# Kernel optimization log

Measured on AMD Instinct MI355X. Metric: run time of the kernel, lower is better.

Reference implementation:

```python
import jax, jax.numpy as jnp
import numpy as np

N_HEADS = 12
ROPE_THETA = 10000.0


def _rope(x, pos):
    # x: [B, H, S, hd]; rotate only first hd//2 channels (partial RoPE, dim=head_dim//2)
    rot = x.shape[-1] // 2
    inv_freq = 1.0 / (ROPE_THETA ** (jnp.arange(0, rot, 2, dtype=jnp.float32) / rot))  # [rot/2]
    freqs = pos[:, None] * inv_freq[None, :]          # [S, rot/2]
    freqs = jnp.repeat(freqs, 2, axis=-1)             # [S, rot] interleaved repeat
    cos = jnp.cos(freqs)
    sin = jnp.sin(freqs)
    x_rot, x_pass = x[..., :rot], x[..., rot:]
    xr = x_rot.reshape(x_rot.shape[:-1] + (rot // 2, 2))
    x_half = jnp.stack([-xr[..., 1], xr[..., 0]], axis=-1).reshape(x_rot.shape)
    x_rot = x_rot * cos + x_half * sin
    return jnp.concatenate([x_rot, x_pass], axis=-1)


def setup_inputs() -> dict:
    key = jax.random.key(0)
    ks = jax.random.split(key, 9)
    B, S, D = 2, 2048, 768
    x = jax.random.normal(ks[0], (B, S, D), dtype=jnp.float32)
    w = lambda k: jax.random.normal(k, (D, D), dtype=jnp.float32) * 0.02
    return {
        'x': x,
        'Wq': w(ks[1]), 'bq': jnp.zeros((D,), jnp.float32),
        'Wk': w(ks[2]), 'bk': jnp.zeros((D,), jnp.float32),
        'Wv': w(ks[3]), 'bv': jnp.zeros((D,), jnp.float32),
        'Wo': w(ks[4]), 'bo': jnp.zeros((D,), jnp.float32),
    }


def reference(x, Wq, bq, Wk, bk, Wv, bv, Wo, bo):
    B, S, D = x.shape
    H = N_HEADS
    hd = D // H
    # QKV projections (torch Linear: y = x W^T + b)
    q = (x @ Wq.T + bq).reshape(B, S, H, hd).transpose(0, 2, 1, 3)  # [B,H,S,hd]
    k = (x @ Wk.T + bk).reshape(B, S, H, hd).transpose(0, 2, 1, 3)
    v = (x @ Wv.T + bv).reshape(B, S, H, hd).transpose(0, 2, 1, 3)
    pos = jnp.arange(S, dtype=jnp.float32)
    q = _rope(q, pos)
    k = _rope(k, pos)
    scale = 1.0 / jnp.sqrt(jnp.asarray(hd, jnp.float32))
    scores = jnp.einsum('bhqd,bhkd->bhqk', q, k) * scale            # [B,H,S,S]
    causal = jnp.tril(jnp.ones((S, S), dtype=bool))
    scores = jnp.where(causal, scores, jnp.finfo(scores.dtype).min)
    attn = jax.nn.softmax(scores, axis=-1)
    out = jnp.einsum('bhqk,bhkd->bhqd', attn, v)                    # [B,H,S,hd]
    out = out.transpose(0, 2, 1, 3).reshape(B, S, D)
    return out @ Wo.T + bo
```

## Files before the change

kernel.cpp:

```cpp
#include <hip/hip_runtime.h>
#include <math.h>

#define S_  2048
#define D_  768
#define H_  12

typedef float f32x4 __attribute__((ext_vector_type(4)));
typedef __bf16 bf16x8 __attribute__((ext_vector_type(8)));
typedef unsigned short u16;

#define MFMA(a, b, c) __builtin_amdgcn_mfma_f32_16x16x32_bf16(a, b, c, 0, 0, 0)
#define LOG2E 1.44269504f

__device__ __forceinline__ u16 f2bf(float f) {
  union { float f; unsigned u; } c;
  c.f = f;
  unsigned r = c.u + 0x7FFFu + ((c.u >> 16) & 1u);
  return (u16)(r >> 16);
}

typedef const unsigned int __attribute__((address_space(1))) gu32;
typedef unsigned int __attribute__((address_space(3))) lu32;

__device__ __forceinline__ void gload_lds16(const void* g, void* l) {
  __builtin_amdgcn_global_load_lds((gu32*)g, (lu32*)l, 16, 0, 0);
}

__global__ __launch_bounds__(256) void trig_kernel(float2* __restrict__ trig) {
  int i = blockIdx.x * 256 + threadIdx.x;
  int s = i >> 4, p = i & 15;
  float inv = powf(10000.0f, -(float)p / 16.0f);
  float f = (float)s * inv;
  trig[i] = make_float2(cosf(f), sinf(f));
}

__global__ __launch_bounds__(256) void cvt_all(
    const float* __restrict__ x, const float* __restrict__ wq,
    const float* __restrict__ wk, const float* __restrict__ wv,
    const float* __restrict__ wo, u16* __restrict__ xb, u16* __restrict__ wqb,
    u16* __restrict__ wkb, u16* __restrict__ wvb, u16* __restrict__ wob) {
  int idx = blockIdx.x * 256 + threadIdx.x;
  const float4* src;
  u16* dst;
  int off;
  if (idx < 786432) {
    src = (const float4*)x; dst = xb; off = idx;
  } else {
    int r = idx - 786432;
    int sel = r / 147456;
    off = r - sel * 147456;
    src = (const float4*)(sel == 0 ? wq : sel == 1 ? wk : sel == 2 ? wv : wo);
    dst = sel == 0 ? wqb : sel == 1 ? wkb : sel == 2 ? wvb : wob;
  }
  float4 v = src[off];
  ushort4 h = make_ushort4(f2bf(v.x), f2bf(v.y), f2bf(v.z), f2bf(v.w));
  *(ushort4*)(dst + (size_t)off * 4) = h;
}

template <int MODE>
__global__ __launch_bounds__(256) void proj_mfma(
    const u16* __restrict__ A, const u16* __restrict__ Wb,
    const float* __restrict__ bias, void* __restrict__ dst,
    const float2* __restrict__ trig) {
  __shared__ u16 As[4096];
  __shared__ u16 Bs[4096];
  const int t = threadIdx.x;
  const int l = t & 63, w = t >> 6;
  const int wr = w >> 1, wc = w & 1;
  const int n0 = blockIdx.x * 64;
  const int m0 = blockIdx.y * 64;

  const f32x4 zero = {0.f, 0.f, 0.f, 0.f};
  f32x4 acc[2][2];
#pragma unroll
  for (int i = 0; i < 2; ++i)
#pragma unroll
    for (int j = 0; j < 2; ++j) acc[i][j] = zero;

  for (int k0 = 0; k0 < 768; k0 += 64) {
    __syncthreads();
#pragma unroll
    for (int rnd = 0; rnd < 2; ++rnd) {
      int id = t + rnd * 256;
      int r = id >> 3, c = id & 7;
      int cs = ((c ^ (r & 7)) << 3);
      gload_lds16(A + (size_t)(m0 + r) * 768 + k0 + cs,
                  &As[(w * 64 + rnd * 256) * 8]);
      gload_lds16(Wb + (size_t)(n0 + r) * 768 + k0 + cs,
                  &Bs[(w * 64 + rnd * 256) * 8]);
    }
    __syncthreads();

    bf16x8 af[2][2], bw[2][2];
#pragma unroll
    for (int mf = 0; mf < 2; ++mf)
#pragma unroll
      for (int kh = 0; kh < 2; ++kh) {
        int row = wr * 32 + mf * 16 + (l & 15);
        int ch = (kh * 4 + (l >> 4)) ^ (row & 7);
        af[mf][kh] = *(const bf16x8*)&As[row * 64 + ch * 8];
      }
#pragma unroll
    for (int nf = 0; nf < 2; ++nf)
#pragma unroll
      for (int kh = 0; kh < 2; ++kh) {
        int row = wc * 32 + nf * 16 + (l & 15);
        int ch = (kh * 4 + (l >> 4)) ^ (row & 7);
        bw[nf][kh] = *(const bf16x8*)&Bs[row * 64 + ch * 8];
      }
#pragma unroll
    for (int kh = 0; kh < 2; ++kh)
#pragma unroll
      for (int mf = 0; mf < 2; ++mf)
#pragma unroll
        for (int nf = 0; nf < 2; ++nf)
          acc[mf][nf] = MFMA(af[mf][kh], bw[nf][kh], acc[mf][nf]);
  }

  const int b_ = m0 >> 11;
  const int h = n0 >> 6;
#pragma unroll
  for (int mf = 0; mf < 2; ++mf) {
    const int rbase = m0 + wr * 32 + mf * 16 + ((l >> 4) << 2);
#pragma unroll
    for (int nf = 0; nf < 2; ++nf) {
      const int col = wc * 32 + nf * 16 + (l & 15);
      const int n = n0 + col;
      const float bia = bias[n];
      f32x4 v = acc[mf][nf];
      if (MODE == 0) {
        float* out = (float*)dst;
#pragma unroll
        for (int g = 0; g < 4; ++g)
          out[(size_t)(rbase + g) * 768 + n] = v[g] + bia;
      } else if (MODE == 1) {
        u16* o = (u16*)dst;
        const int d = col;
#pragma unroll
        for (int g = 0; g < 4; ++g) {
          float val = v[g] + bia;
          float partner = __shfl_xor(val, 1);
          if (d < 32) {
            int s = (rbase + g) & (S_ - 1);
            float2 cs = trig[s * 16 + (d >> 1)];
            val = (d & 1) ? (val * cs.x + partner * cs.y)
                          : (val * cs.x - partner * cs.y);
          }
          o[((size_t)(b_ * H_ + h) * S_ + ((rbase + g) & (S_ - 1))) * 64 + d] =
              f2bf(val);
        }
      } else {
        u16* o = (u16*)dst;
        const int d = col;
        ushort4 pk;
        pk.x = f2bf(v[0] + bia);
        pk.y = f2bf(v[1] + bia);
        pk.z = f2bf(v[2] + bia);
        pk.w = f2bf(v[3] + bia);
        *(ushort4*)&o[((size_t)(b_ * H_ + h) * 64 + d) * S_ +
                      (rbase & (S_ - 1))] = pk;
      }
    }
  }
}

__global__ __launch_bounds__(256) void attn_mfma(
    const u16* __restrict__ qg, const u16* __restrict__ kg,
    const u16* __restrict__ vtg, u16* __restrict__ ctx) {
  __shared__ u16 Ks[4096];
  __shared__ u16 Vts[4096];
  __shared__ u16 Ps[4096];
  const int t = threadIdx.x, l = t & 63, w = t >> 6;

  int orig = blockIdx.y * 32 + blockIdx.x;
  int logical = (orig & 7) * 96 + (orig >> 3);
  const int bh = logical >> 5;
  const int qt = 31 - (logical & 31);
  const int q0 = qt * 64;

  const u16* qp = qg + (size_t)bh * (S_ * 64);
  const u16* kp = kg + (size_t)bh * (S_ * 64);
  const u16* vp = vtg + (size_t)bh * (64 * S_);

  bf16x8 aq[2];
  {
    const u16* qrow = qp + (size_t)(q0 + w * 16 + (l & 15)) * 64 + ((l >> 4) * 8);
    aq[0] = *(const bf16x8*)(qrow);
    aq[1] = *(const bf16x8*)(qrow + 32);
  }

  const f32x4 zero = {0.f, 0.f, 0.f, 0.f};
  f32x4 o[4];
  float m_r[4], l_r[4];
#pragma unroll
  for (int i = 0; i < 4; ++i) {
    o[i] = zero;
    m_r[i] = -3.0e38f;
    l_r[i] = 0.f;
  }

  for (int kt = 0; kt <= qt; ++kt) {
    const int k0 = kt * 64;
    __syncthreads();
#pragma unroll
    for (int rnd = 0; rnd < 2; ++rnd) {
      int id = t + rnd * 256;
      int r = id >> 3, c = id & 7;
      int cs = ((c ^ (r & 7)) << 3);
      gload_lds16(kp + (size_t)(k0 + r) * 64 + cs, &Ks[(w * 64 + rnd * 256) * 8]);
      gload_lds16(vp + (size_t)r * S_ + k0 + cs, &Vts[(w * 64 + rnd * 256) * 8]);
    }
    __syncthreads();

    f32x4 sacc[4];
#pragma unroll
    for (int ks = 0; ks < 4; ++ks) sacc[ks] = zero;
#pragma unroll
    for (int ks = 0; ks < 4; ++ks)
#pragma unroll
      for (int kh = 0; kh < 2; ++kh) {
        int row = ks * 16 + (l & 15);
        int ch = (kh * 4 + (l >> 4)) ^ (row & 7);
        bf16x8 bk = *(const bf16x8*)&Ks[row * 64 + ch * 8];
        sacc[ks] = MFMA(aq[kh], bk, sacc[ks]);
      }

    const int prow_b = w * 16 + ((l >> 4) << 2);
    const int qrow_b = q0 + prow_b;
#pragma unroll
    for (int g = 0; g < 4; ++g) {
      const int qrow = qrow_b + g;
      float sv[4], mx = -3.0e38f;
#pragma unroll
      for (int ks = 0; ks < 4; ++ks) {
        int kcol = k0 + ks * 16 + (l & 15);
        float xv = sacc[ks][g] * 0.125f;
        if (kcol > qrow) xv = -3.0e38f;
        sv[ks] = xv;
        mx = fmaxf(mx, xv);
      }
#pragma unroll
      for (int off = 1; off < 16; off <<= 1)
        mx = fmaxf(mx, __shfl_xor(mx, off));
      float mnew = fmaxf(m_r[g], mx);
      float corr = __expf(m_r[g] - mnew);
      m_r[g] = mnew;
      float rs = 0.f;
      const int prow = prow_b + g;
      const int swz = (prow & 7) << 4;
#pragma unroll
      for (int ks = 0; ks < 4; ++ks) {
        float p = __expf(sv[ks] - mnew);
        rs += p;
        int byt = (ks * 32 + ((l & 15) * 2)) ^ swz;
        Ps[prow * 64 + (byt >> 1)] = f2bf(p);
      }
#pragma unroll
      for (int off = 1; off < 16; off <<= 1) rs += __shfl_xor(rs, off);
      l_r[g] = l_r[g] * corr + rs;
#pragma unroll
      for (int ds = 0; ds < 4; ++ds) o[ds][g] *= corr;
    }

#pragma unroll
    for (int kh = 0; kh < 2; ++kh) {
      int prow = w * 16 + (l & 15);
      int ch = (kh * 4 + (l >> 4)) ^ (prow & 7);
      bf16x8 pa = *(const bf16x8*)&Ps[prow * 64 + ch * 8];
#pragma unroll
      for (int ds = 0; ds < 4; ++ds) {
        int vrow = ds * 16 + (l & 15);
        int vch = (kh * 4 + (l >> 4)) ^ (vrow & 7);
        bf16x8 vb = *(const bf16x8*)&Vts[vrow * 64 + vch * 8];
        o[ds] = MFMA(pa, vb, o[ds]);
      }
    }
  }

  const int b_ = bh / H_, h = bh - b_ * H_;
#pragma unroll
  for (int g = 0; g < 4; ++g) {
    const int q = q0 + w * 16 + ((l >> 4) << 2) + g;
    const float inv = 1.0f / l_r[g];
#pragma unroll
    for (int ds = 0; ds < 4; ++ds)
      ctx[((size_t)(b_ * S_ + q)) * 768 + h * 64 + ds * 16 + (l & 15)] =
          f2bf(o[ds][g] * inv);
  }
}

extern "C" void kernel_launch(void* const* d_in, const int* in_sizes, int n_in,
                              void* d_out, int out_size, void* d_ws,
                              size_t ws_size, hipStream_t stream) {
  const float* x = (const float*)d_in[0];
  const float* Wq = (const float*)d_in[1];
  const float* bq = (const float*)d_in[2];
  const float* Wk = (const float*)d_in[3];
  const float* bk = (const float*)d_in[4];
  const float* Wv = (const float*)d_in[5];
  const float* bv = (const float*)d_in[6];
  const float* Wo = (const float*)d_in[7];
  const float* bo = (const float*)d_in[8];

  char* p = (char*)d_ws;
  float2* trig = (float2*)p;          p += (size_t)32768 * sizeof(float2);
  u16* xb = (u16*)p;                  p += (size_t)3145728 * 2;
  u16* wqb = (u16*)p;                 p += (size_t)589824 * 2;
  u16* wkb = (u16*)p;                 p += (size_t)589824 * 2;
  u16* wvb = (u16*)p;                 p += (size_t)589824 * 2;
  u16* wob = (u16*)p;                 p += (size_t)589824 * 2;
  u16* qb = (u16*)p;                  p += (size_t)3145728 * 2;
  u16* kb = (u16*)p;                  p += (size_t)3145728 * 2;
  u16* vtb = (u16*)p;                 p += (size_t)3145728 * 2;
  u16* ctxb = (u16*)p;                p += (size_t)3145728 * 2;

  cvt_all<<<5376, 256, 0, stream>>>(x, Wq, Wk, Wv, Wo, xb, wqb, wkb, wvb, wob);
  trig_kernel<<<128, 256, 0, stream>>>(trig);

  dim3 pgrid(12, 64);
  proj_mfma<1><<<pgrid, 256, 0, stream>>>(xb, wqb, bq, qb, trig);
  proj_mfma<1><<<pgrid, 256, 0, stream>>>(xb, wkb, bk, kb, trig);
  proj_mfma<3><<<pgrid, 256, 0, stream>>>(xb, wvb, bv, vtb, nullptr);

  attn_mfma<<<dim3(32, 24), 256, 0, stream>>>(qb, kb, vtb, ctxb);

  proj_mfma<0><<<pgrid, 256, 0, stream>>>(ctxb, wob, bo, d_out, nullptr);
}
```

Measured before the change: 223.7 us.

## Double-buffer K/V tiles in attention and skip rescale when max is stable

The attention kernel now double-buffers the K and V^T tiles in LDS. It issues the async load of the next tile before computing the current one and drops one of the two barriers per iteration. It also adds a lazy online-softmax rescale: the output and running sum are corrected only when some row's new max exceeds the stored max by more than a threshold. This costs extra LDS, which may reduce occupancy. Deferring the max update bounds exp arguments but lets probabilities exceed 1 before bf16 conversion.

```diff
diff --git a/kernel.cpp b/kernel.cpp
--- a/kernel.cpp
+++ b/kernel.cpp
@@ -167,8 +167,8 @@
 __global__ __launch_bounds__(256) void attn_mfma(
     const u16* __restrict__ qg, const u16* __restrict__ kg,
     const u16* __restrict__ vtg, u16* __restrict__ ctx) {
-  __shared__ u16 Ks[4096];
-  __shared__ u16 Vts[4096];
+  __shared__ u16 Ks[2][4096];
+  __shared__ u16 Vts[2][4096];
   __shared__ u16 Ps[4096];
   const int t = threadIdx.x, l = t & 63, w = t >> 6;
 
@@ -182,6 +182,20 @@
   const u16* kp = kg + (size_t)bh * (S_ * 64);
   const u16* vp = vtg + (size_t)bh * (64 * S_);
 
+#define STAGE(kt_, buf_)                                                      \
+  {                                                                           \
+    const int k0s = (kt_)*64;                                                 \
+    _Pragma("unroll") for (int rnd = 0; rnd < 2; ++rnd) {                     \
+      int id = t + rnd * 256;                                                 \
+      int r = id >> 3, c = id & 7;                                            \
+      int cs = ((c ^ (r & 7)) << 3);                                          \
+      gload_lds16(kp + (size_t)(k0s + r) * 64 + cs,                           \
+                  &Ks[buf_][(w * 64 + rnd * 256) * 8]);                       \
+      gload_lds16(vp + (size_t)r * S_ + k0s + cs,                             \
+                  &Vts[buf_][(w * 64 + rnd * 256) * 8]);                      \
+    }                                                                         \
+  }
+
   bf16x8 aq[2];
   {
     const u16* qrow = qp + (size_t)(q0 + w * 16 + (l & 15)) * 64 + ((l >> 4) * 8);
@@ -199,18 +213,13 @@
     l_r[i] = 0.f;
   }
 
+  STAGE(0, 0);
+  __syncthreads();
+
   for (int kt = 0; kt <= qt; ++kt) {
     const int k0 = kt * 64;
-    __syncthreads();
-#pragma unroll
-    for (int rnd = 0; rnd < 2; ++rnd) {
-      int id = t + rnd * 256;
-      int r = id >> 3, c = id & 7;
-      int cs = ((c ^ (r & 7)) << 3);
-      gload_lds16(kp + (size_t)(k0 + r) * 64 + cs, &Ks[(w * 64 + rnd * 256) * 8]);
-      gload_lds16(vp + (size_t)r * S_ + k0 + cs, &Vts[(w * 64 + rnd * 256) * 8]);
-    }
-    __syncthreads();
+    const int cur = kt & 1;
+    if (kt < qt) STAGE(kt + 1, cur ^ 1);
 
     f32x4 sacc[4];
 #pragma unroll
@@ -221,7 +230,7 @@
       for (int kh = 0; kh < 2; ++kh) {
         int row = ks * 16 + (l & 15);
         int ch = (kh * 4 + (l >> 4)) ^ (row & 7);
-        bf16x8 bk = *(const bf16x8*)&Ks[row * 64 + ch * 8];
+        bf16x8 bk = *(const bf16x8*)&Ks[cur][row * 64 + ch * 8];
         sacc[ks] = MFMA(aq[kh], bk, sacc[ks]);
       }
 
@@ -230,36 +239,40 @@
 #pragma unroll
     for (int g = 0; g < 4; ++g) {
       const int qrow = qrow_b + g;
-      float sv[4], mx = -3.0e38f;
+      float sv[4];
 #pragma unroll
       for (int ks = 0; ks < 4; ++ks) {
         int kcol = k0 + ks * 16 + (l & 15);
         float xv = sacc[ks][g] * 0.125f;
         if (kcol > qrow) xv = -3.0e38f;
         sv[ks] = xv;
-        mx = fmaxf(mx, xv);
-      }
+      }
+      float mx = fmaxf(fmaxf(sv[0], sv[1]), fmaxf(sv[2], sv[3]));
 #pragma unroll
       for (int off = 1; off < 16; off <<= 1)
         mx = fmaxf(mx, __shfl_xor(mx, off));
-      float mnew = fmaxf(m_r[g], mx);
-      float corr = __expf(m_r[g] - mnew);
-      m_r[g] = mnew;
+      float c = 1.f;
+      if (!__all(mx <= m_r[g] + 8.f)) {
+        float mnew = fmaxf(m_r[g], mx);
+        c = __expf(m_r[g] - mnew);
+        m_r[g] = mnew;
+#pragma unroll
+        for (int ds = 0; ds < 4; ++ds) o[ds][g] *= c;
+      }
+      const float mm = m_r[g];
       float rs = 0.f;
       const int prow = prow_b + g;
       const int swz = (prow & 7) << 4;
 #pragma unroll
       for (int ks = 0; ks < 4; ++ks) {
-        float p = __expf(sv[ks] - mnew);
+        float p = __expf(sv[ks] - mm);
         rs += p;
         int byt = (ks * 32 + ((l & 15) * 2)) ^ swz;
         Ps[prow * 64 + (byt >> 1)] = f2bf(p);
       }
 #pragma unroll
       for (int off = 1; off < 16; off <<= 1) rs += __shfl_xor(rs, off);
-      l_r[g] = l_r[g] * corr + rs;
-#pragma unroll
-      for (int ds = 0; ds < 4; ++ds) o[ds][g] *= corr;
+      l_r[g] = l_r[g] * c + rs;
     }
 
 #pragma unroll
@@ -271,11 +284,14 @@
       for (int ds = 0; ds < 4; ++ds) {
         int vrow = ds * 16 + (l & 15);
         int vch = (kh * 4 + (l >> 4)) ^ (vrow & 7);
-        bf16x8 vb = *(const bf16x8*)&Vts[vrow * 64 + vch * 8];
+        bf16x8 vb = *(const bf16x8*)&Vts[cur][vrow * 64 + vch * 8];
         o[ds] = MFMA(pa, vb, o[ds]);
       }
     }
-  }
+
+    __syncthreads();
+  }
+#undef STAGE
 
   const int b_ = bh / H_, h = bh - b_ * H_;
 #pragma unroll
```

Result: no change. 222.3 us (-0.6%).
